# Kernel optimization log

Measured on AMD Instinct MI355X. Metric: run time of the kernel, lower is better.

The kernel has to match this reference:

```python
import jax, jax.numpy as jnp
import numpy as np
import math

B, H, S, D = 2, 8, 1024, 384
LAMBDA_INIT = 0.8 - 0.6 * math.exp(-0.3 * 1)  # depth = 1


def _clin(xr, xi, wr, wi, br=None, bi=None):
    # complex linear: (xr + i xi) @ (wr + i wi)^T + (br + i bi)
    o_r = jnp.einsum('bhse,de->bhsd', xr, wr) - jnp.einsum('bhse,de->bhsd', xi, wi)
    o_i = jnp.einsum('bhse,de->bhsd', xr, wi) + jnp.einsum('bhse,de->bhsd', xi, wr)
    if br is not None:
        o_r = o_r + br
        o_i = o_i + bi
    return o_r, o_i


def _attn_w(qr, qi, kr, ki, scale):
    # complex score magnitude -> softmax
    s_r = jnp.einsum('bhqd,bhkd->bhqk', qr, kr) + jnp.einsum('bhqd,bhkd->bhqk', qi, ki)
    s_i = jnp.einsum('bhqd,bhkd->bhqk', qi, kr) - jnp.einsum('bhqd,bhkd->bhqk', qr, ki)
    return jax.nn.softmax(jnp.sqrt(s_r ** 2 + s_i ** 2 + 1e-8) * scale, axis=-1)


def setup_inputs() -> dict:
    key = jax.random.key(0)
    ks = jax.random.split(key, 32)
    n = lambda k, sh, std=1.0: jax.random.normal(k, sh, dtype=jnp.float32) * std
    sd = 1.0 / math.sqrt(D)
    inp = {
        'q_r': n(ks[0], (B, H, S, D)), 'q_i': n(ks[1], (B, H, S, D)),
        'k_r': n(ks[2], (B, H, S, D)), 'k_i': n(ks[3], (B, H, S, D)),
        'v_r': n(ks[4], (B, H, S, D)), 'v_i': n(ks[5], (B, H, S, D)),
        'pe_q_r': n(ks[6], (B, H, S, D)), 'pe_q_i': n(ks[7], (B, H, S, D)),
        'pe_k_r': n(ks[8], (B, H, S, D)), 'pe_k_i': n(ks[9], (B, H, S, D)),
        'wq_r': n(ks[10], (2 * D, D), sd), 'wq_i': n(ks[11], (2 * D, D), sd),
        'bq_r': jnp.zeros((2 * D,), jnp.float32), 'bq_i': jnp.zeros((2 * D,), jnp.float32),
        'wk_r': n(ks[12], (D, D), sd), 'wk_i': n(ks[13], (D, D), sd),
        'bk_r': jnp.zeros((D,), jnp.float32), 'bk_i': jnp.zeros((D,), jnp.float32),
        'wv_r': n(ks[14], (D, D), sd), 'wv_i': n(ks[15], (D, D), sd),
        'bv_r': jnp.zeros((D,), jnp.float32), 'bv_i': jnp.zeros((D,), jnp.float32),
        'wg_r': n(ks[16], (D, D), sd), 'wg_i': n(ks[17], (D, D), sd),
        'bg_r': jnp.zeros((D,), jnp.float32), 'bg_i': jnp.zeros((D,), jnp.float32),
        'wo_r': n(ks[18], (D, D), sd), 'wo_i': n(ks[19], (D, D), sd),
        'bo_r': jnp.zeros((D,), jnp.float32), 'bo_i': jnp.zeros((D,), jnp.float32),
        'lam_q1': n(ks[20], (D,), 0.1), 'lam_k1': n(ks[21], (D,), 0.1),
        'lam_q2': n(ks[22], (D,), 0.1), 'lam_k2': n(ks[23], (D,), 0.1),
        'subln_w': jnp.ones((2 * D,), jnp.float32),
    }
    return inp


def reference(q_r, q_i, k_r, k_i, v_r, v_i, pe_q_r, pe_q_i, pe_k_r, pe_k_i,
              wq_r, wq_i, bq_r, bq_i, wk_r, wk_i, bk_r, bk_i,
              wv_r, wv_i, bv_r, bv_i, wg_r, wg_i, bg_r, bg_i,
              wo_r, wo_i, bo_r, bo_i, lam_q1, lam_k1, lam_q2, lam_k2, subln_w):
    scale = D ** (-0.5)
    qp_r, qp_i = _clin(q_r, q_i, wq_r, wq_i, bq_r, bq_i)   # [B,H,S,2D]
    kp_r, kp_i = _clin(k_r, k_i, wk_r, wk_i, bk_r, bk_i)   # [B,H,S,D]
    vp_r, vp_i = _clin(v_r, v_i, wv_r, wv_i, bv_r, bv_i)
    qp_r = qp_r + jnp.concatenate([pe_q_r, pe_q_r], axis=-1)
    qp_i = qp_i + jnp.concatenate([pe_q_i, pe_q_i], axis=-1)
    kp_r = kp_r + pe_k_r
    kp_i = kp_i + pe_k_i
    q1_r, q2_r = jnp.split(qp_r, 2, axis=-1)
    q1_i, q2_i = jnp.split(qp_i, 2, axis=-1)
    w1 = _attn_w(q1_r, q1_i, kp_r, kp_i, scale)
    w2 = _attn_w(q2_r, q2_i, kp_r, kp_i, scale)
    a1_r = jnp.einsum('bhqk,bhkd->bhqd', w1, vp_r)
    a1_i = jnp.einsum('bhqk,bhkd->bhqd', w1, vp_i)
    a2_r = jnp.einsum('bhqk,bhkd->bhqd', w2, vp_r)
    a2_i = jnp.einsum('bhqk,bhkd->bhqd', w2, vp_i)
    cat_r = jnp.concatenate([a1_r, a2_r], axis=-1)
    cat_i = jnp.concatenate([a1_i, a2_i], axis=-1)
    # complex RMSNorm (SubLN) over 2D dim
    rms = jnp.sqrt(jnp.mean(cat_r ** 2 + cat_i ** 2, axis=-1, keepdims=True) + 1e-5)
    cat_r = cat_r / rms * subln_w
    cat_i = cat_i / rms * subln_w
    a1_r, a2_r = jnp.split(cat_r, 2, axis=-1)
    a1_i, a2_i = jnp.split(cat_i, 2, axis=-1)
    lam1 = jnp.exp(jnp.sum(lam_q1 * lam_k1))
    lam2 = jnp.exp(jnp.sum(lam_q2 * lam_k2))
    lam = jax.nn.sigmoid(lam1 - lam2 + LAMBDA_INIT)
    out_r = a1_r - lam * a2_r
    out_i = a1_i - lam * a2_i
    g_r, g_i = _clin(q_r, q_i, wg_r, wg_i, bg_r, bg_i)
    out_r, out_i = g_r * out_r - g_i * out_i, g_r * out_i + g_i * out_r
    out_r, out_i = _clin(out_r, out_i, wo_r, wo_i, bo_r, bo_i)
    return (out_r, out_i)
```

## Files before the change

kernel.cpp:

```cpp
#include <hip/hip_runtime.h>
#include <cstdint>


typedef _Float16 f16;
typedef __attribute__((ext_vector_type(8))) _Float16 f16x8;
typedef __attribute__((ext_vector_type(4))) _Float16 f16x4;
typedef __attribute__((ext_vector_type(4))) float    f32x4;

#define NROW      16384L
#define HALF_OUT  6291456L
#define SCALE_QK  0.05103103630798288f
#define LAMBDA_INIT 0.35550906759096926f

__device__ __forceinline__ void gl2lds16(const void* g, void* l) {
  __builtin_amdgcn_global_load_lds(
      (const __attribute__((address_space(1))) void*)(uintptr_t)g,
      (__attribute__((address_space(3))) void*)(uint32_t)(uintptr_t)l,
      16, 0, 0);
}

struct PeTab { const float* p[6]; float sgn[6]; };

enum { MODE_PROJ = 0, MODE_VT = 1, MODE_OUT = 2, MODE_PV = 3 };

template <int MODE>
__launch_bounds__(512, 2)
__global__ void gemm256(const f16* __restrict__ A, int lda,
                        const f16* __restrict__ W, int ldw,
                        const float* __restrict__ bias, PeTab pe,
                        void* __restrict__ outp, void* __restrict__ outp2,
                        int ldo, int K, int gx)
{
  __shared__ f16 As[2][256 * 64];
  __shared__ f16 Bs[2][256 * 64];
  const int t    = threadIdx.x;
  const int lane = t & 63;
  const int wave = t >> 6;
  const int bid  = blockIdx.x;
  const int xcd  = bid & 7;
  const int per  = bid >> 3;

  long row0, col0;
  const f16 *Ab, *Wb;
  int bh = 0;
  if (MODE == MODE_PV) {
    const int pd3 = per / 3;
    const int ntile = per - pd3 * 3;
    const int mt_g = xcd * 16 + pd3;
    bh   = mt_g >> 3;
    row0 = (long)(mt_g & 7) * 256;
    col0 = (long)ntile * 256;
    Ab = A + ((long)(bh + (row0 >= 1024 ? 16 : 0)) << 20) + (row0 & 1023) * (long)lda;
    Wb = W + (long)bh * 768 * 1024 + col0 * (long)ldw;
  } else {
    row0 = (long)(xcd * 8 + per / gx) * 256;
    col0 = (long)(per % gx) * 256;
    Ab = A + row0 * (long)lda;
    Wb = W + col0 * (long)ldw;
  }

  const int wm = (wave >> 2) * 128;
  const int wn = (wave & 3) * 64;
  const int lm = lane & 15;
  const int l4 = lane >> 4;

  f32x4 acc[8][4] = {};

  auto stage = [&](int kk, int sub) {
#pragma unroll
    for (int p = 0; p < 4; ++p) {
      int sg = p * 512 + t;
      int r = sg >> 3, cl = sg & 7;
      int cg = cl ^ (r & 7);
      gl2lds16(Ab + (long)r * lda + kk + cg * 8, &As[sub][sg * 8]);
      gl2lds16(Wb + (long)r * ldw + kk + cg * 8, &Bs[sub][sg * 8]);
    }
  };

  const int NT = K >> 6;
  stage(0, 0);
  stage(64, 1);
  int cur = 0;
  for (int it = 0; it < NT; ++it) {
    if (it + 1 < NT) asm volatile("s_waitcnt vmcnt(8)" ::: "memory");
    else             asm volatile("s_waitcnt vmcnt(0)" ::: "memory");
    __builtin_amdgcn_s_barrier();
#pragma unroll
    for (int ks = 0; ks < 2; ++ks) {
      f16x8 bfr[4];
#pragma unroll
      for (int nt = 0; nt < 4; ++nt) {
        int rr = wn + nt * 16 + lm;
        bfr[nt] = *(const f16x8*)&Bs[cur][rr * 64 + (((ks * 4 + l4) ^ (rr & 7)) * 8)];
      }
#pragma unroll
      for (int mt = 0; mt < 8; ++mt) {
        int rr = wm + mt * 16 + lm;
        f16x8 afr = *(const f16x8*)&As[cur][rr * 64 + (((ks * 4 + l4) ^ (rr & 7)) * 8)];
#pragma unroll
        for (int nt = 0; nt < 4; ++nt)
          acc[mt][nt] = __builtin_amdgcn_mfma_f32_16x16x32_f16(afr, bfr[nt], acc[mt][nt], 0, 0, 0);
      }
    }
    __builtin_amdgcn_s_barrier();
    if (it + 2 < NT) stage((it + 2) << 6, cur);
    cur ^= 1;
  }

  const int lm4 = l4 * 4;
  const int ln  = lm;
#pragma unroll
  for (int mt = 0; mt < 8; ++mt) {
#pragma unroll
    for (int nt = 0; nt < 4; ++nt) {
      int col = (int)col0 + wn + nt * 16 + ln;
      if (MODE == MODE_VT) {
        long rowb = row0 + wm + mt * 16 + lm4;
        long vbh = rowb >> 10, sx = rowb & 1023;
        f16x4 v;
#pragma unroll
        for (int r = 0; r < 4; ++r) v[r] = (f16)(acc[mt][nt][r] + bias[col]);
        *(f16x4*)&((f16*)outp)[(vbh * 768 + col) * 1024 + sx] = v;
      } else if (MODE == MODE_PV) {
#pragma unroll
        for (int r = 0; r < 4; ++r) {
          long grow = row0 + wm + mt * 16 + lm4 + r;
          f16 val = (f16)acc[mt][nt][r];
          if (grow < 1024) ((f16*)outp )[((long)bh * 1024 + grow)        * 768 + col] = val;
          else             ((f16*)outp2)[((long)bh * 1024 + grow - 1024) * 768 + col] = val;
        }
      } else {
#pragma unroll
        for (int r = 0; r < 4; ++r) {
          long row = row0 + wm + mt * 16 + lm4 + r;
          float c = acc[mt][nt][r] + bias[col];
          if (MODE == MODE_PROJ) {
            int s2 = col / 384;
            int d  = col - s2 * 384;
            const float* pp = pe.p[s2];
            if (pp) c += pe.sgn[s2] * pp[row * 384 + d];
            ((f16*)outp)[row * (long)ldo + col] = (f16)c;
          } else {
            float* of = (float*)outp;
            if (col < 384) of[row * 384 + col] = c;
            else           of[HALF_OUT + row * 384 + (col - 384)] = c;
          }
        }
      }
    }
  }
}

__launch_bounds__(512, 2)
__global__ void score256(const f16* __restrict__ QG, const f16* __restrict__ Kc,
                         f16* __restrict__ P)
{
  __shared__ f16 As[2][256 * 64];
  __shared__ f16 Bs[2][128 * 64];
  __shared__ f16 Cs[2][128 * 64];
  const int t = threadIdx.x, lane = t & 63, wave = t >> 6;
  const int bid = blockIdx.x;
  const int xcd = bid & 7, per = bid >> 3;
  const int slab = xcd * 4 + (per >> 5);
  const int tile = per & 31;
  const int w = slab >> 4, bh = slab & 15;
  const long row0 = (long)(tile >> 3) * 256;
  const long col0 = (long)(tile & 7) * 128;
  const f16* Ab = QG + (long)bh * 1024 * 2304 + row0 * 2304 + w * 768;
  const f16* Bb = Kc + (long)bh * 1024 * 768 + col0 * 768;

  const int wm = (wave >> 1) * 64;
  const int wn = (wave & 1) * 64;
  const int lm = lane & 15, l4 = lane >> 4;

  f32x4 accr[4][4] = {}, acci[4][4] = {};

  auto stage = [&](int kk, int sub) {
    int kk2 = kk < 384 ? kk + 384 : kk - 384;
#pragma unroll
    for (int p = 0; p < 4; ++p) {
      int sg = p * 512 + t;
      int r = sg >> 3, cl = sg & 7, cg = cl ^ (r & 7);
      gl2lds16(Ab + (long)r * 2304 + kk + cg * 8, &As[sub][sg * 8]);
    }
#pragma unroll
    for (int p = 0; p < 2; ++p) {
      int sg = p * 512 + t;
      int r = sg >> 3, cl = sg & 7, cg = cl ^ (r & 7);
      gl2lds16(Bb + (long)r * 768 + kk  + cg * 8, &Bs[sub][sg * 8]);
      gl2lds16(Bb + (long)r * 768 + kk2 + cg * 8, &Cs[sub][sg * 8]);
    }
  };

  stage(0, 0);
  stage(64, 1);
  int cur = 0;
  for (int it = 0; it < 12; ++it) {
    if (it + 1 < 12) asm volatile("s_waitcnt vmcnt(8)" ::: "memory");
    else             asm volatile("s_waitcnt vmcnt(0)" ::: "memory");
    __builtin_amdgcn_s_barrier();
    const bool neg = (it < 6);
#pragma unroll
    for (int ks = 0; ks < 2; ++ks) {
      f16x8 bfr[4], cfr[4];
#pragma unroll
      for (int nt = 0; nt < 4; ++nt) {
        int rr = wn + nt * 16 + lm;
        int off = rr * 64 + (((ks * 4 + l4) ^ (rr & 7)) * 8);
        bfr[nt] = *(const f16x8*)&Bs[cur][off];
        cfr[nt] = *(const f16x8*)&Cs[cur][off];
      }
#pragma unroll
      for (int mt = 0; mt < 4; ++mt) {
        int rr = wm + mt * 16 + lm;
        f16x8 a  = *(const f16x8*)&As[cur][rr * 64 + (((ks * 4 + l4) ^ (rr & 7)) * 8)];
        f16x8 am = neg ? -a : a;
#pragma unroll
        for (int nt = 0; nt < 4; ++nt) {
          accr[mt][nt] = __builtin_amdgcn_mfma_f32_16x16x32_f16(a,  bfr[nt], accr[mt][nt], 0, 0, 0);
          acci[mt][nt] = __builtin_amdgcn_mfma_f32_16x16x32_f16(am, cfr[nt], acci[mt][nt], 0, 0, 0);
        }
      }
    }
    __builtin_amdgcn_s_barrier();
    if (it + 2 < 12) stage((it + 2) << 6, cur);
    cur ^= 1;
  }

  f16* Pz = P + ((long)slab << 20);
  const int lm4 = l4 * 4, ln = lm;
#pragma unroll
  for (int mt = 0; mt < 4; ++mt)
#pragma unroll
    for (int nt = 0; nt < 4; ++nt) {
      int col = (int)col0 + wn + nt * 16 + ln;
#pragma unroll
      for (int r = 0; r < 4; ++r) {
        long row = row0 + wm + mt * 16 + lm4 + r;
        float sr = accr[mt][nt][r], si = acci[mt][nt][r];
        float m = sqrtf(sr * sr + si * si + 1e-8f) * SCALE_QK;
        Pz[row * 1024 + col] = (f16)m;
      }
    }
}

__global__ void softmax_kernel(f16* __restrict__ P)
{
  const long row = (long)blockIdx.x * 4 + (threadIdx.x >> 6);
  f16* p = P + row * 1024;
  const int lane = threadIdx.x & 63;
  f16x8 v0 = *(const f16x8*)(p + lane * 16);
  f16x8 v1 = *(const f16x8*)(p + lane * 16 + 8);
  float x[16];
#pragma unroll
  for (int i = 0; i < 8; ++i) { x[i] = (float)v0[i]; x[8 + i] = (float)v1[i]; }
  float m = x[0];
#pragma unroll
  for (int i = 1; i < 16; ++i) m = fmaxf(m, x[i]);
#pragma unroll
  for (int off = 1; off < 64; off <<= 1) m = fmaxf(m, __shfl_xor(m, off));
  float s = 0.f;
#pragma unroll
  for (int i = 0; i < 16; ++i) { x[i] = __expf(x[i] - m); s += x[i]; }
#pragma unroll
  for (int off = 1; off < 64; off <<= 1) s += __shfl_xor(s, off);
  float inv = 1.f / s;
  f16x8 o0, o1;
#pragma unroll
  for (int i = 0; i < 8; ++i) { o0[i] = (f16)(x[i] * inv); o1[i] = (f16)(x[8 + i] * inv); }
  *(f16x8*)(p + lane * 16)     = o0;
  *(f16x8*)(p + lane * 16 + 8) = o1;
}

__global__ void fuse_kernel(const f16* __restrict__ A1, const f16* __restrict__ A2,
                            const f16* __restrict__ QG, const float* __restrict__ subw,
                            const float* __restrict__ lamp, f16* __restrict__ Xatt)
{
  const long row = blockIdx.x;
  const int t = threadIdx.x, lane = t & 63, wv = t >> 6;
  const f16* a1 = A1 + row * 768;
  const f16* a2 = A2 + row * 768;
  const f16* g  = QG + row * 2304 + 1536;
  float a1r[3], a1i[3], a2r[3], a2i[3];
  float ss = 0.f;
#pragma unroll
  for (int q = 0; q < 3; ++q) {
    int d = t + q * 128;
    a1r[q] = (float)a1[d]; a1i[q] = (float)a1[d + 384];
    a2r[q] = (float)a2[d]; a2i[q] = (float)a2[d + 384];
    ss += a1r[q] * a1r[q] + a1i[q] * a1i[q] + a2r[q] * a2r[q] + a2i[q] * a2i[q];
  }
#pragma unroll
  for (int m = 1; m < 64; m <<= 1) ss += __shfl_xor(ss, m);
  __shared__ float part[2];
  if (lane == 0) part[wv] = ss;
  __syncthreads();
  float inv = rsqrtf((part[0] + part[1]) * (1.f / 768.f) + 1e-5f);
  float lam = lamp[0];
#pragma unroll
  for (int q = 0; q < 3; ++q) {
    int d = t + q * 128;
    float w1 = subw[d], w2 = subw[d + 384];
    float n1r = a1r[q] * inv * w1, n1i = a1i[q] * inv * w1;
    float n2r = a2r[q] * inv * w2, n2i = a2i[q] * inv * w2;
    float orr = n1r - lam * n2r, oii = n1i - lam * n2i;
    float gr = (float)g[d], gi = (float)g[d + 384];
    Xatt[row * 768 + d]       = (f16)(gr * orr - gi * oii);
    Xatt[row * 768 + d + 384] = (f16)(gr * oii + gi * orr);
  }
}

__global__ void lam_kernel(const float* lq1, const float* lk1,
                           const float* lq2, const float* lk2, float* out)
{
  const int t = threadIdx.x, lane = t & 63, wv = t >> 6;
  float s1 = 0.f, s2 = 0.f;
#pragma unroll
  for (int q = 0; q < 3; ++q) {
    int d = t + q * 128;
    s1 += lq1[d] * lk1[d];
    s2 += lq2[d] * lk2[d];
  }
#pragma unroll
  for (int m = 1; m < 64; m <<= 1) { s1 += __shfl_xor(s1, m); s2 += __shfl_xor(s2, m); }
  __shared__ float p1[2], p2[2];
  if (lane == 0) { p1[wv] = s1; p2[wv] = s2; }
  __syncthreads();
  if (t == 0) {
    float x = expf(p1[0] + p1[1]) - expf(p2[0] + p2[1]) + LAMBDA_INIT;
    out[0] = 1.f / (1.f + expf(-x));
  }
}

__global__ void pack_x(const float* __restrict__ xr, const float* __restrict__ xi,
                       f16* __restrict__ X)
{
  long i = (long)blockIdx.x * 256 + threadIdx.x;
  long row = i / 96;
  int  rem = (int)(i - row * 96);
  int  c   = rem * 8;
  const float* src = (c < 384) ? (xr + row * 384 + c) : (xi + row * 384 + (c - 384));
  f16x8 o;
#pragma unroll
  for (int j = 0; j < 8; ++j) o[j] = (f16)src[j];
  *(f16x8*)&X[row * 768 + c] = o;
}

__global__ void pack_wq(const float* wq_r, const float* wq_i,
                        const float* wg_r, const float* wg_i,
                        const float* bq_r, const float* bq_i,
                        const float* bg_r, const float* bg_i,
                        f16* __restrict__ Wp, float* __restrict__ bp)
{
  long i = (long)blockIdx.x * 256 + threadIdx.x;
  int n = (int)(i / 768), e = (int)(i % 768);
  int s = n / 384, d = n - s * 384;
  int hb = (e >= 384);
  int ee = e - hb * 384;
  float v = 0.f, b = 0.f;
  switch (s) {
    case 0: v = hb ? -wq_i[d * 384 + ee]         :  wq_r[d * 384 + ee];         b = bq_r[d];       break;
    case 1: v = hb ?  wq_r[d * 384 + ee]         :  wq_i[d * 384 + ee];         b = bq_i[d];       break;
    case 2: v = hb ? -wq_i[(384 + d) * 384 + ee] :  wq_r[(384 + d) * 384 + ee]; b = bq_r[384 + d]; break;
    case 3: v = hb ?  wq_r[(384 + d) * 384 + ee] :  wq_i[(384 + d) * 384 + ee]; b = bq_i[384 + d]; break;
    case 4: v = hb ? -wg_i[d * 384 + ee]         :  wg_r[d * 384 + ee];         b = bg_r[d];       break;
    case 5: v = hb ?  wg_r[d * 384 + ee]         :  wg_i[d * 384 + ee];         b = bg_i[d];       break;
  }
  Wp[i] = (f16)v;
  if (e == 0) bp[n] = b;
}

__global__ void pack_w_std(const float* wr, const float* wi,
                           const float* br, const float* bi,
                           f16* __restrict__ Wp, float* __restrict__ bp)
{
  long i = (long)blockIdx.x * 256 + threadIdx.x;
  int n = (int)(i / 768), e = (int)(i % 768);
  int hb = (e >= 384);
  int ee = e - hb * 384;
  float v, b;
  if (n < 384) { v = hb ? -wi[n * 384 + ee] : wr[n * 384 + ee]; b = br[n]; }
  else { int d = n - 384; v = hb ? wr[d * 384 + ee] : wi[d * 384 + ee]; b = bi[d]; }
  Wp[i] = (f16)v;
  if (e == 0) bp[n] = b;
}

extern "C" void kernel_launch(void* const* d_in, const int* in_sizes, int n_in,
                              void* d_out, int out_size, void* d_ws, size_t ws_size,
                              hipStream_t stream)
{
  const float* q_r    = (const float*)d_in[0];
  const float* q_i    = (const float*)d_in[1];
  const float* k_r    = (const float*)d_in[2];
  const float* k_i    = (const float*)d_in[3];
  const float* v_r    = (const float*)d_in[4];
  const float* v_i    = (const float*)d_in[5];
  const float* pe_q_r = (const float*)d_in[6];
  const float* pe_q_i = (const float*)d_in[7];
  const float* pe_k_r = (const float*)d_in[8];
  const float* pe_k_i = (const float*)d_in[9];
  const float* wq_r = (const float*)d_in[10];
  const float* wq_i = (const float*)d_in[11];
  const float* bq_r = (const float*)d_in[12];
  const float* bq_i = (const float*)d_in[13];
  const float* wk_r = (const float*)d_in[14];
  const float* wk_i = (const float*)d_in[15];
  const float* bk_r = (const float*)d_in[16];
  const float* bk_i = (const float*)d_in[17];
  const float* wv_r = (const float*)d_in[18];
  const float* wv_i = (const float*)d_in[19];
  const float* bv_r = (const float*)d_in[20];
  const float* bv_i = (const float*)d_in[21];
  const float* wg_r = (const float*)d_in[22];
  const float* wg_i = (const float*)d_in[23];
  const float* bg_r = (const float*)d_in[24];
  const float* bg_i = (const float*)d_in[25];
  const float* wo_r = (const float*)d_in[26];
  const float* wo_i = (const float*)d_in[27];
  const float* bo_r = (const float*)d_in[28];
  const float* bo_i = (const float*)d_in[29];
  const float* lam_q1 = (const float*)d_in[30];
  const float* lam_k1 = (const float*)d_in[31];
  const float* lam_q2 = (const float*)d_in[32];
  const float* lam_k2 = (const float*)d_in[33];
  const float* subln_w = (const float*)d_in[34];

  char* base = (char*)d_ws;
  size_t off = 0;
  auto alloc = [&](size_t bytes) -> void* {
    void* p = base + off;
    off = (off + bytes + 255) & ~(size_t)255;
    return p;
  };
  f16*   Wq   = (f16*)alloc(2304L * 768 * 2);
  f16*   Wk   = (f16*)alloc(768L * 768 * 2);
  f16*   Wv   = (f16*)alloc(768L * 768 * 2);
  f16*   Wo   = (f16*)alloc(768L * 768 * 2);
  float* bq   = (float*)alloc(2304 * 4);
  float* bk   = (float*)alloc(768 * 4);
  float* bv   = (float*)alloc(768 * 4);
  float* bo   = (float*)alloc(768 * 4);
  float* lamp = (float*)alloc(4);
  f16*   X    = (f16*)alloc(NROW * 768 * 2);
  f16*   QG   = (f16*)alloc(NROW * 2304 * 2);
  f16*   Kc   = (f16*)alloc(NROW * 768 * 2);
  f16*   Vt   = (f16*)alloc(16L * 768 * 1024 * 2);
  f16*   P    = (f16*)alloc(32L * 1024 * 1024 * 2);
  if (off > ws_size) return;
  f16* A1   = Kc;
  f16* A2   = X;
  f16* Xatt = Vt;

  pack_wq<<<6912, 256, 0, stream>>>(wq_r, wq_i, wg_r, wg_i, bq_r, bq_i, bg_r, bg_i, Wq, bq);
  pack_w_std<<<2304, 256, 0, stream>>>(wk_r, wk_i, bk_r, bk_i, Wk, bk);
  pack_w_std<<<2304, 256, 0, stream>>>(wv_r, wv_i, bv_r, bv_i, Wv, bv);
  pack_w_std<<<2304, 256, 0, stream>>>(wo_r, wo_i, bo_r, bo_i, Wo, bo);
  lam_kernel<<<1, 128, 0, stream>>>(lam_q1, lam_k1, lam_q2, lam_k2, lamp);

  PeTab pe0{};

  pack_x<<<6144, 256, 0, stream>>>(q_r, q_i, X);
  PeTab peQ{};
  peQ.p[0] = pe_q_r; peQ.sgn[0] = 1.f;
  peQ.p[1] = pe_q_i; peQ.sgn[1] = 1.f;
  peQ.p[2] = pe_q_r; peQ.sgn[2] = 1.f;
  peQ.p[3] = pe_q_i; peQ.sgn[3] = 1.f;
  gemm256<MODE_PROJ><<<576, 512, 0, stream>>>(
      X, 768, Wq, 768, bq, peQ, QG, nullptr, 2304, 768, 9);

  pack_x<<<6144, 256, 0, stream>>>(k_r, k_i, X);
  PeTab peK{};
  peK.p[0] = pe_k_r; peK.sgn[0] = 1.f;
  peK.p[1] = pe_k_i; peK.sgn[1] = 1.f;
  gemm256<MODE_PROJ><<<192, 512, 0, stream>>>(
      X, 768, Wk, 768, bk, peK, Kc, nullptr, 768, 768, 3);

  pack_x<<<6144, 256, 0, stream>>>(v_r, v_i, X);
  gemm256<MODE_VT><<<192, 512, 0, stream>>>(
      X, 768, Wv, 768, bv, pe0, Vt, nullptr, 0, 768, 3);

  score256<<<1024, 512, 0, stream>>>(QG, Kc, P);
  softmax_kernel<<<8192, 256, 0, stream>>>(P);
  gemm256<MODE_PV><<<384, 512, 0, stream>>>(
      P, 1024, Vt, 1024, nullptr, pe0, A1, A2, 0, 1024, 0);

  fuse_kernel<<<16384, 128, 0, stream>>>(A1, A2, QG, subln_w, lamp, Xatt);

  gemm256<MODE_OUT><<<192, 512, 0, stream>>>(
      Xatt, 768, Wo, 768, bo, pe0, d_out, nullptr, 0, 768, 3);

  (void)in_sizes; (void)n_in; (void)out_size;
}
```

Before: 854.5 us.

## Shrink GEMM and score tiles to 128x128 and pre-pack positional encodings to fp16

Replaces the 256-wide GEMM and score kernels with 128x128-tile, 256-thread versions, which quadruples or doubles the grid so more blocks run concurrently on the GPU. The score kernel now splits the real and imaginary K halves into separate LDS buffers and runs four MFMAs per step over a 32-wide K slice. Positional-encoding inputs are packed once into fp16 scratch (reusing the P buffer) and added in the projection epilogue through a column limit, replacing the fp32 pointer-table lookups. Smaller tiles give less operand reuse per block and more total global traffic, and fp16 PE adds a little rounding error.

```diff
diff --git a/kernel.cpp b/kernel.cpp
--- a/kernel.cpp
+++ b/kernel.cpp
@@ -19,20 +19,19 @@
       16, 0, 0);
 }
 
-struct PeTab { const float* p[6]; float sgn[6]; };
-
 enum { MODE_PROJ = 0, MODE_VT = 1, MODE_OUT = 2, MODE_PV = 3 };
 
 template <int MODE>
-__launch_bounds__(512, 2)
-__global__ void gemm256(const f16* __restrict__ A, int lda,
+__launch_bounds__(256, 2)
+__global__ void gemm128(const f16* __restrict__ A, int lda,
                         const f16* __restrict__ W, int ldw,
-                        const float* __restrict__ bias, PeTab pe,
+                        const float* __restrict__ bias,
+                        const f16* __restrict__ pe16, int pelim,
                         void* __restrict__ outp, void* __restrict__ outp2,
                         int ldo, int K, int gx)
 {
-  __shared__ f16 As[2][256 * 64];
-  __shared__ f16 Bs[2][256 * 64];
+  __shared__ f16 As[2][128 * 64];
+  __shared__ f16 Bs[2][128 * 64];
   const int t    = threadIdx.x;
   const int lane = t & 63;
   const int wave = t >> 6;
@@ -44,34 +43,32 @@
   const f16 *Ab, *Wb;
   int bh = 0;
   if (MODE == MODE_PV) {
-    const int pd3 = per / 3;
-    const int ntile = per - pd3 * 3;
-    const int mt_g = xcd * 16 + pd3;
-    bh   = mt_g >> 3;
-    row0 = (long)(mt_g & 7) * 256;
-    col0 = (long)ntile * 256;
-    Ab = A + ((long)(bh + (row0 >= 1024 ? 16 : 0)) << 20) + (row0 & 1023) * (long)lda;
+    bh = xcd * 2 + per / 96;
+    const int rem = per % 96;
+    row0 = (long)(rem / 6) * 128;
+    col0 = (long)(rem % 6) * 128;
+    const int slab = bh + (row0 >= 1024 ? 16 : 0);
+    Ab = A + ((long)slab << 20) + (row0 & 1023) * (long)lda;
     Wb = W + (long)bh * 768 * 1024 + col0 * (long)ldw;
   } else {
-    row0 = (long)(xcd * 8 + per / gx) * 256;
-    col0 = (long)(per % gx) * 256;
+    row0 = (long)(xcd * 16 + per / gx) * 128;
+    col0 = (long)(per % gx) * 128;
     Ab = A + row0 * (long)lda;
     Wb = W + col0 * (long)ldw;
   }
 
-  const int wm = (wave >> 2) * 128;
-  const int wn = (wave & 3) * 64;
+  const int wm = (wave >> 1) * 64;
+  const int wn = (wave & 1) * 64;
   const int lm = lane & 15;
   const int l4 = lane >> 4;
 
-  f32x4 acc[8][4] = {};
+  f32x4 acc[4][4] = {};
 
   auto stage = [&](int kk, int sub) {
 #pragma unroll
     for (int p = 0; p < 4; ++p) {
-      int sg = p * 512 + t;
-      int r = sg >> 3, cl = sg & 7;
-      int cg = cl ^ (r & 7);
+      int sg = p * 256 + t;
+      int r = sg >> 3, cl = sg & 7, cg = cl ^ (r & 7);
       gl2lds16(Ab + (long)r * lda + kk + cg * 8, &As[sub][sg * 8]);
       gl2lds16(Wb + (long)r * ldw + kk + cg * 8, &Bs[sub][sg * 8]);
     }
@@ -91,12 +88,12 @@
 #pragma unroll
       for (int nt = 0; nt < 4; ++nt) {
         int rr = wn + nt * 16 + lm;
-        bfr[nt] = *(const f16x8*)&Bs[cur][rr * 64 + (((ks * 4 + l4) ^ (rr & 7)) * 8)];
+        bfr[nt] = *(const f16x8*)&Bs[cur][rr * 64 + (((ks * 4 + l4) ^ (rr & 7)) << 3)];
       }
 #pragma unroll
-      for (int mt = 0; mt < 8; ++mt) {
+      for (int mt = 0; mt < 4; ++mt) {
         int rr = wm + mt * 16 + lm;
-        f16x8 afr = *(const f16x8*)&As[cur][rr * 64 + (((ks * 4 + l4) ^ (rr & 7)) * 8)];
+        f16x8 afr = *(const f16x8*)&As[cur][rr * 64 + (((ks * 4 + l4) ^ (rr & 7)) << 3)];
 #pragma unroll
         for (int nt = 0; nt < 4; ++nt)
           acc[mt][nt] = __builtin_amdgcn_mfma_f32_16x16x32_f16(afr, bfr[nt], acc[mt][nt], 0, 0, 0);
@@ -110,7 +107,7 @@
   const int lm4 = l4 * 4;
   const int ln  = lm;
 #pragma unroll
-  for (int mt = 0; mt < 8; ++mt) {
+  for (int mt = 0; mt < 4; ++mt) {
 #pragma unroll
     for (int nt = 0; nt < 4; ++nt) {
       int col = (int)col0 + wn + nt * 16 + ln;
@@ -135,10 +132,10 @@
           long row = row0 + wm + mt * 16 + lm4 + r;
           float c = acc[mt][nt][r] + bias[col];
           if (MODE == MODE_PROJ) {
-            int s2 = col / 384;
-            int d  = col - s2 * 384;
-            const float* pp = pe.p[s2];
-            if (pp) c += pe.sgn[s2] * pp[row * 384 + d];
+            if (col < pelim) {
+              int pc = col < 768 ? col : col - 768;
+              c += (float)pe16[row * 768 + pc];
+            }
             ((f16*)outp)[row * (long)ldo + col] = (f16)c;
           } else {
             float* of = (float*)outp;
@@ -151,83 +148,73 @@
   }
 }
 
-__launch_bounds__(512, 2)
-__global__ void score256(const f16* __restrict__ QG, const f16* __restrict__ Kc,
+__launch_bounds__(256, 2)
+__global__ void score128(const f16* __restrict__ QG, const f16* __restrict__ Kc,
                          f16* __restrict__ P)
 {
-  __shared__ f16 As[2][256 * 64];
-  __shared__ f16 Bs[2][128 * 64];
-  __shared__ f16 Cs[2][128 * 64];
+  __shared__ f16 AsL[2][128 * 32], AsH[2][128 * 32];
+  __shared__ f16 BsL[2][128 * 32], BsH[2][128 * 32];
   const int t = threadIdx.x, lane = t & 63, wave = t >> 6;
   const int bid = blockIdx.x;
   const int xcd = bid & 7, per = bid >> 3;
-  const int slab = xcd * 4 + (per >> 5);
-  const int tile = per & 31;
-  const int w = slab >> 4, bh = slab & 15;
-  const long row0 = (long)(tile >> 3) * 256;
-  const long col0 = (long)(tile & 7) * 128;
-  const f16* Ab = QG + (long)bh * 1024 * 2304 + row0 * 2304 + w * 768;
-  const f16* Bb = Kc + (long)bh * 1024 * 768 + col0 * 768;
-
-  const int wm = (wave >> 1) * 64;
-  const int wn = (wave & 1) * 64;
+  const int z   = xcd * 4 + per / 64;
+  const int rem = per % 64;
+  const int w = z >> 4, bh = z & 15;
+  const long row0 = (long)(rem / 8) * 128, col0 = (long)(rem % 8) * 128;
+  const f16* A = QG + (long)bh * 1024 * 2304 + row0 * 2304 + w * 768;
+  const f16* B = Kc + (long)bh * 1024 * 768 + col0 * 768;
+  f16* Pz = P + ((long)z << 20);
+
+  const int wm = (wave >> 1) * 64, wn = (wave & 1) * 64;
   const int lm = lane & 15, l4 = lane >> 4;
-
   f32x4 accr[4][4] = {}, acci[4][4] = {};
 
   auto stage = [&](int kk, int sub) {
-    int kk2 = kk < 384 ? kk + 384 : kk - 384;
-#pragma unroll
-    for (int p = 0; p < 4; ++p) {
-      int sg = p * 512 + t;
-      int r = sg >> 3, cl = sg & 7, cg = cl ^ (r & 7);
-      gl2lds16(Ab + (long)r * 2304 + kk + cg * 8, &As[sub][sg * 8]);
-    }
 #pragma unroll
     for (int p = 0; p < 2; ++p) {
-      int sg = p * 512 + t;
-      int r = sg >> 3, cl = sg & 7, cg = cl ^ (r & 7);
-      gl2lds16(Bb + (long)r * 768 + kk  + cg * 8, &Bs[sub][sg * 8]);
-      gl2lds16(Bb + (long)r * 768 + kk2 + cg * 8, &Cs[sub][sg * 8]);
+      int sg = p * 256 + t;
+      int r = sg >> 2, cl = sg & 3, cg = cl ^ (r & 3);
+      gl2lds16(A + (long)r * 2304 + kk + cg * 8,       &AsL[sub][sg * 8]);
+      gl2lds16(A + (long)r * 2304 + 384 + kk + cg * 8, &AsH[sub][sg * 8]);
+      gl2lds16(B + (long)r * 768 + kk + cg * 8,        &BsL[sub][sg * 8]);
+      gl2lds16(B + (long)r * 768 + 384 + kk + cg * 8,  &BsH[sub][sg * 8]);
     }
   };
 
   stage(0, 0);
-  stage(64, 1);
+  stage(32, 1);
   int cur = 0;
   for (int it = 0; it < 12; ++it) {
     if (it + 1 < 12) asm volatile("s_waitcnt vmcnt(8)" ::: "memory");
     else             asm volatile("s_waitcnt vmcnt(0)" ::: "memory");
     __builtin_amdgcn_s_barrier();
-    const bool neg = (it < 6);
-#pragma unroll
-    for (int ks = 0; ks < 2; ++ks) {
-      f16x8 bfr[4], cfr[4];
+    f16x8 bl[4], bh2[4];
+#pragma unroll
+    for (int nt = 0; nt < 4; ++nt) {
+      int rr = wn + nt * 16 + lm;
+      int off = rr * 32 + (((l4 ^ (rr & 3))) << 3);
+      bl[nt]  = *(const f16x8*)&BsL[cur][off];
+      bh2[nt] = *(const f16x8*)&BsH[cur][off];
+    }
+#pragma unroll
+    for (int mt = 0; mt < 4; ++mt) {
+      int rr = wm + mt * 16 + lm;
+      int off = rr * 32 + (((l4 ^ (rr & 3))) << 3);
+      f16x8 al  = *(const f16x8*)&AsL[cur][off];
+      f16x8 ah  = *(const f16x8*)&AsH[cur][off];
+      f16x8 nal = -al;
 #pragma unroll
       for (int nt = 0; nt < 4; ++nt) {
-        int rr = wn + nt * 16 + lm;
-        int off = rr * 64 + (((ks * 4 + l4) ^ (rr & 7)) * 8);
-        bfr[nt] = *(const f16x8*)&Bs[cur][off];
-        cfr[nt] = *(const f16x8*)&Cs[cur][off];
+        accr[mt][nt] = __builtin_amdgcn_mfma_f32_16x16x32_f16(al,  bl[nt],  accr[mt][nt], 0, 0, 0);
+        accr[mt][nt] = __builtin_amdgcn_mfma_f32_16x16x32_f16(ah,  bh2[nt], accr[mt][nt], 0, 0, 0);
+        acci[mt][nt] = __builtin_amdgcn_mfma_f32_16x16x32_f16(ah,  bl[nt],  acci[mt][nt], 0, 0, 0);
+        acci[mt][nt] = __builtin_amdgcn_mfma_f32_16x16x32_f16(nal, bh2[nt], acci[mt][nt], 0, 0, 0);
       }
-#pragma unroll
-      for (int mt = 0; mt < 4; ++mt) {
-        int rr = wm + mt * 16 + lm;
-        f16x8 a  = *(const f16x8*)&As[cur][rr * 64 + (((ks * 4 + l4) ^ (rr & 7)) * 8)];
-        f16x8 am = neg ? -a : a;
-#pragma unroll
-        for (int nt = 0; nt < 4; ++nt) {
-          accr[mt][nt] = __builtin_amdgcn_mfma_f32_16x16x32_f16(a,  bfr[nt], accr[mt][nt], 0, 0, 0);
-          acci[mt][nt] = __builtin_amdgcn_mfma_f32_16x16x32_f16(am, cfr[nt], acci[mt][nt], 0, 0, 0);
-        }
-      }
     }
     __builtin_amdgcn_s_barrier();
-    if (it + 2 < 12) stage((it + 2) << 6, cur);
+    if (it + 2 < 12) stage((it + 2) << 5, cur);
     cur ^= 1;
   }
-
-  f16* Pz = P + ((long)slab << 20);
   const int lm4 = l4 * 4, ln = lm;
 #pragma unroll
   for (int mt = 0; mt < 4; ++mt)
@@ -450,44 +437,38 @@
   f16* A1   = Kc;
   f16* A2   = X;
   f16* Xatt = Vt;
+  f16* PEQ  = P;
+  f16* PEK  = P + NROW * 768;
 
   pack_wq<<<6912, 256, 0, stream>>>(wq_r, wq_i, wg_r, wg_i, bq_r, bq_i, bg_r, bg_i, Wq, bq);
   pack_w_std<<<2304, 256, 0, stream>>>(wk_r, wk_i, bk_r, bk_i, Wk, bk);
   pack_w_std<<<2304, 256, 0, stream>>>(wv_r, wv_i, bv_r, bv_i, Wv, bv);
   pack_w_std<<<2304, 256, 0, stream>>>(wo_r, wo_i, bo_r, bo_i, Wo, bo);
   lam_kernel<<<1, 128, 0, stream>>>(lam_q1, lam_k1, lam_q2, lam_k2, lamp);
-
-  PeTab pe0{};
+  pack_x<<<6144, 256, 0, stream>>>(pe_q_r, pe_q_i, PEQ);
+  pack_x<<<6144, 256, 0, stream>>>(pe_k_r, pe_k_i, PEK);
 
   pack_x<<<6144, 256, 0, stream>>>(q_r, q_i, X);
-  PeTab peQ{};
-  peQ.p[0] = pe_q_r; peQ.sgn[0] = 1.f;
-  peQ.p[1] = pe_q_i; peQ.sgn[1] = 1.f;
-  peQ.p[2] = pe_q_r; peQ.sgn[2] = 1.f;
-  peQ.p[3] = pe_q_i; peQ.sgn[3] = 1.f;
-  gemm256<MODE_PROJ><<<576, 512, 0, stream>>>(
-      X, 768, Wq, 768, bq, peQ, QG, nullptr, 2304, 768, 9);
+  gemm128<MODE_PROJ><<<2304, 256, 0, stream>>>(
+      X, 768, Wq, 768, bq, PEQ, 1536, QG, nullptr, 2304, 768, 18);
 
   pack_x<<<6144, 256, 0, stream>>>(k_r, k_i, X);
-  PeTab peK{};
-  peK.p[0] = pe_k_r; peK.sgn[0] = 1.f;
-  peK.p[1] = pe_k_i; peK.sgn[1] = 1.f;
-  gemm256<MODE_PROJ><<<192, 512, 0, stream>>>(
-      X, 768, Wk, 768, bk, peK, Kc, nullptr, 768, 768, 3);
+  gemm128<MODE_PROJ><<<768, 256, 0, stream>>>(
+      X, 768, Wk, 768, bk, PEK, 768, Kc, nullptr, 768, 768, 6);
 
   pack_x<<<6144, 256, 0, stream>>>(v_r, v_i, X);
-  gemm256<MODE_VT><<<192, 512, 0, stream>>>(
-      X, 768, Wv, 768, bv, pe0, Vt, nullptr, 0, 768, 3);
-
-  score256<<<1024, 512, 0, stream>>>(QG, Kc, P);
+  gemm128<MODE_VT><<<768, 256, 0, stream>>>(
+      X, 768, Wv, 768, bv, nullptr, 0, Vt, nullptr, 0, 768, 6);
+
+  score128<<<2048, 256, 0, stream>>>(QG, Kc, P);
   softmax_kernel<<<8192, 256, 0, stream>>>(P);
-  gemm256<MODE_PV><<<384, 512, 0, stream>>>(
-      P, 1024, Vt, 1024, nullptr, pe0, A1, A2, 0, 1024, 0);
+  gemm128<MODE_PV><<<1536, 256, 0, stream>>>(
+      P, 1024, Vt, 1024, nullptr, nullptr, 0, A1, A2, 0, 1024, 0);
 
   fuse_kernel<<<16384, 128, 0, stream>>>(A1, A2, QG, subln_w, lamp, Xatt);
 
-  gemm256<MODE_OUT><<<192, 512, 0, stream>>>(
-      Xatt, 768, Wo, 768, bo, pe0, d_out, nullptr, 0, 768, 3);
+  gemm128<MODE_OUT><<<768, 256, 0, stream>>>(
+      Xatt, 768, Wo, 768, bo, nullptr, 0, d_out, nullptr, 0, 768, 6);
 
   (void)in_sizes; (void)n_in; (void)out_size;
 }
```

Result: faster. 763.4 us (-10.7%).
